# Optimization experiments

Hardware: AMD Instinct MI355X
Metric: run time of the kernel (lower is better)

Reference implementation:

```python
import jax, jax.numpy as jnp
import numpy as np

TEMPERATURE = 0.07
B, D = 8192, 256

def _l2norm(x, axis=-1, eps=1e-12):
    # matches torch F.normalize(p=2): x / max(||x||, eps)
    n = jnp.sqrt(jnp.sum(x * x, axis=axis, keepdims=True))
    return x / jnp.maximum(n, eps)

def setup_inputs() -> dict:
    key = jax.random.key(0)
    k1, k2, k3 = jax.random.split(key, 3)
    return {
        "h_emb": jax.random.normal(k1, (B, D), dtype=jnp.float32),
        "r_emb": jax.random.normal(k2, (B, D), dtype=jnp.float32),
        "t_emb": jax.random.normal(k3, (B, D), dtype=jnp.float32),
    }

def reference(h_emb, r_emb, t_emb):
    # query = normalize(h + r); positives/negatives = normalize(t)
    q = _l2norm(h_emb + r_emb, axis=1)          # [B, D]
    t = _l2norm(t_emb, axis=1)                  # [B, D]
    # Dense in-batch similarity. The original builds logits = [pos, off-diag negs];
    # since the diagonal of sim IS the positive similarity, cross-entropy with
    # label 0 equals logsumexp over the full row minus the diagonal entry.
    sim = jnp.einsum('bd,nd->bn', q, t) / TEMPERATURE   # [B, B]
    pos = jnp.diagonal(sim)                              # [B]
    loss = jnp.mean(jax.nn.logsumexp(sim, axis=1) - pos)
    return loss
```

## Files before the change

### kernel.cpp

```cpp
#include <hip/hip_runtime.h>
#include <hip/hip_bf16.h>

#define B_DIM 8192
#define D_DIM 256
#define GRID_GEMM 512
#define NT 16

constexpr float INV_T = 14.285714285714286f;

typedef __bf16 bf16x8 __attribute__((ext_vector_type(8)));
typedef float  f32x16 __attribute__((ext_vector_type(16)));

#define GLOBAL_U32(p) ((const __attribute__((address_space(1))) unsigned int*)(p))
#define LDS_U32(p)    ((__attribute__((address_space(3))) unsigned int*)(p))

#define WAITCNT_VM8 0x0F78

__device__ inline unsigned short f2bf(float f) {
    union { float f; unsigned u; } x; x.f = f;
    unsigned r = x.u + 0x7fffu + ((x.u >> 16) & 1u);
    return (unsigned short)(r >> 16);
}

__global__ __launch_bounds__(256) void norm_kernel(
    const float* __restrict__ h, const float* __restrict__ r,
    const float* __restrict__ t,
    unsigned short* __restrict__ qws, unsigned short* __restrict__ tws,
    float* __restrict__ rowsum, float* __restrict__ diagsum, int* __restrict__ ticket)
{
    if (blockIdx.x == 0) {
        float4* rs4 = (float4*)rowsum;
#pragma unroll
        for (int i = 0; i < 8; ++i)
            rs4[threadIdx.x * 8 + i] = make_float4(0.f, 0.f, 0.f, 0.f);
        if (threadIdx.x == 0) { *diagsum = 0.f; *ticket = 0; }
    }

    int wave = threadIdx.x >> 6;
    int lane = threadIdx.x & 63;
    int task = blockIdx.x * 4 + wave;
    bool isQ = task < B_DIM;
    int row  = isQ ? task : task - B_DIM;

    float4 v;
    if (isQ) {
        float4 a = ((const float4*)h)[row * 64 + lane];
        float4 b = ((const float4*)r)[row * 64 + lane];
        v = make_float4(a.x + b.x, a.y + b.y, a.z + b.z, a.w + b.w);
    } else {
        v = ((const float4*)t)[row * 64 + lane];
    }
    float s = v.x * v.x + v.y * v.y + v.z * v.z + v.w * v.w;
#pragma unroll
    for (int off = 32; off; off >>= 1) s += __shfl_xor(s, off, 64);
    float scale = 1.0f / fmaxf(sqrtf(s), 1e-12f);

    ushort4 o;
    o.x = f2bf(v.x * scale);
    o.y = f2bf(v.y * scale);
    o.z = f2bf(v.z * scale);
    o.w = f2bf(v.w * scale);
    ushort4* dst = (ushort4*)(isQ ? qws : tws);
    dst[row * 64 + lane] = o;
}

__global__ __launch_bounds__(256, 2) void gemm_lse_kernel(
    const unsigned char* __restrict__ qws, const unsigned char* __restrict__ tws,
    float* __restrict__ rowsum, float* __restrict__ diagsum,
    int* __restrict__ ticket, float* __restrict__ out)
{
    __shared__ __align__(16) unsigned char ldsB[4][32 * 512];
    __shared__ float wred[4];
    __shared__ int lastflag;

    const int tid  = threadIdx.x;
    const int lane = tid & 63;
    const int w    = tid >> 6;
    const int l31  = lane & 31;
    const int hi   = lane >> 5;

    const int cc   = blockIdx.x & 15;
    const int rb   = blockIdx.x >> 4;
    const int row0 = rb * 256 + w * 64;
    const int col0 = cc * 512;

    int srel[4];
#pragma unroll
    for (int it = 0; it < 4; ++it) {
        int s = it * 256 + tid;
        int n = s >> 5;
        int kc = (s & 31) ^ (n & 7);
        srel[it] = n * 512 + kc * 16;
    }

#define STAGE(snt, bufi)                                                     \
    {                                                                        \
        const unsigned char* gs = tws + (size_t)(col0 + (snt) * 32) * 512;   \
        _Pragma("unroll")                                                    \
        for (int it = 0; it < 4; ++it)                                       \
            __builtin_amdgcn_global_load_lds(                                \
                GLOBAL_U32(gs + srel[it]),                                   \
                LDS_U32(&ldsB[bufi][(it * 256 + tid) * 16]), 16, 0, 0);      \
    }

    STAGE(0, 0);
    STAGE(1, 1);

    bf16x8 a[2][16];
    {
        const unsigned char* abase = qws + (size_t)(row0 + l31) * 512 + hi * 16;
#pragma unroll
        for (int rt = 0; rt < 2; ++rt)
#pragma unroll
            for (int ks = 0; ks < 16; ++ks)
                a[rt][ks] = *(const bf16x8*)(abase + rt * (32 * 512) + ks * 32);
    }

    f32x16 rowacc[2] = {};
    float diagacc = 0.f;
    const int nsw = l31 & 7;

    for (int nt = 0; nt < NT; ++nt) {
        const int snt = (nt + 2 < NT) ? nt + 2 : NT - 1;
        STAGE(snt, (nt + 2) & 3);

        __builtin_amdgcn_s_waitcnt(WAITCNT_VM8);
        __builtin_amdgcn_s_barrier();

        const unsigned char* bbuf = ldsB[nt & 3];
        f32x16 acc0 = {}, acc1 = {};
#pragma unroll
        for (int ks = 0; ks < 16; ++ks) {
            int kc = ks * 2 + hi;
            bf16x8 b = *(const bf16x8*)(bbuf + l31 * 512 + ((kc ^ nsw) * 16));
            acc0 = __builtin_amdgcn_mfma_f32_32x32x16_bf16(a[0][ks], b, acc0, 0, 0, 0);
            acc1 = __builtin_amdgcn_mfma_f32_32x32x16_bf16(a[1][ks], b, acc1, 0, 0, 0);
        }

#pragma unroll
        for (int g = 0; g < 16; ++g) {
            rowacc[0][g] += __expf(fmaf(acc0[g], INV_T, -INV_T));
            rowacc[1][g] += __expf(fmaf(acc1[g], INV_T, -INV_T));
        }

        const int c0t = col0 + nt * 32;
        if (c0t == row0) {
#pragma unroll
            for (int g = 0; g < 16; ++g) {
                int rm = (g & 3) + 8 * (g >> 2) + 4 * hi;
                if (l31 == rm) diagacc += acc0[g] * INV_T;
            }
        }
        if (c0t == row0 + 32) {
#pragma unroll
            for (int g = 0; g < 16; ++g) {
                int rm = (g & 3) + 8 * (g >> 2) + 4 * hi;
                if (l31 == rm) diagacc += acc1[g] * INV_T;
            }
        }
    }

#pragma unroll
    for (int rt = 0; rt < 2; ++rt)
#pragma unroll
        for (int g = 0; g < 16; ++g) {
            float s = rowacc[rt][g];
            s += __shfl_xor(s, 1, 64);
            s += __shfl_xor(s, 2, 64);
            s += __shfl_xor(s, 4, 64);
            s += __shfl_xor(s, 8, 64);
            s += __shfl_xor(s, 16, 64);
            if (l31 == 0) {
                int grow = row0 + rt * 32 + (g & 3) + 8 * (g >> 2) + 4 * hi;
                atomicAdd(&rowsum[grow], s);
            }
        }

    float dsum = diagacc;
#pragma unroll
    for (int off = 32; off; off >>= 1) dsum += __shfl_xor(dsum, off, 64);
    if (lane == 0 && dsum != 0.f) atomicAdd(diagsum, dsum);

    __syncthreads();
    if (tid == 0) {
        __threadfence();
        int old = __hip_atomic_fetch_add(ticket, 1, __ATOMIC_ACQ_REL,
                                         __HIP_MEMORY_SCOPE_AGENT);
        lastflag = (old == GRID_GEMM - 1);
    }
    __syncthreads();
    if (!lastflag) return;

    float lsum = 0.f;
    for (int rr = tid; rr < B_DIM; rr += 256) {
        float rs = __hip_atomic_load(&rowsum[rr], __ATOMIC_RELAXED,
                                     __HIP_MEMORY_SCOPE_AGENT);
        lsum += __logf(rs);
    }
#pragma unroll
    for (int off = 32; off; off >>= 1) lsum += __shfl_xor(lsum, off, 64);
    if (lane == 0) wred[w] = lsum;
    __syncthreads();
    if (tid == 0) {
        float ds = __hip_atomic_load(diagsum, __ATOMIC_RELAXED,
                                     __HIP_MEMORY_SCOPE_AGENT);
        float total = wred[0] + wred[1] + wred[2] + wred[3]
                    + (float)B_DIM * INV_T
                    - ds;
        out[0] = total / (float)B_DIM;
    }
}

extern "C" void kernel_launch(void* const* d_in, const int* in_sizes, int n_in,
                              void* d_out, int out_size, void* d_ws, size_t ws_size,
                              hipStream_t stream)
{
    const float* h = (const float*)d_in[0];
    const float* r = (const float*)d_in[1];
    const float* t = (const float*)d_in[2];

    unsigned char* ws = (unsigned char*)d_ws;
    unsigned short* qws = (unsigned short*)ws;
    unsigned short* tws = (unsigned short*)(ws + 4u * 1024 * 1024);
    float* rowsum  = (float*)(ws + 8u * 1024 * 1024);
    float* diagsum = (float*)(ws + 8u * 1024 * 1024 + 32u * 1024);
    int*   ticket  = (int*)  (ws + 8u * 1024 * 1024 + 32u * 1024 + 16);

    norm_kernel<<<4096, 256, 0, stream>>>(h, r, t, qws, tws, rowsum, diagsum, ticket);
    gemm_lse_kernel<<<GRID_GEMM, 256, 0, stream>>>(
        (const unsigned char*)qws, (const unsigned char*)tws,
        rowsum, diagsum, ticket, (float*)d_out);
}
```

Measured before the change: 134.0 us.

## Software-pipeline exp epilogue behind next tile's MFMAs and coarsen norm kernel

The GEMM loop is restructured so that the exp/row-sum epilogue for tile n-1 is issued after the MFMAs for tile n, with ping-pong accumulators. This lets transcendental VALU work overlap matrix-core execution. s_setprio is also raised around the compute section. Separately, the norm kernel processes four rows per wave with a quarter of the blocks, cutting launch and block overhead. The cost is extra accumulator registers under a 2-blocks-per-CU launch bound, which could cause spills.

```diff
diff --git a/kernel.cpp b/kernel.cpp
--- a/kernel.cpp
+++ b/kernel.cpp
@@ -36,32 +36,36 @@
         if (threadIdx.x == 0) { *diagsum = 0.f; *ticket = 0; }
     }
 
-    int wave = threadIdx.x >> 6;
-    int lane = threadIdx.x & 63;
-    int task = blockIdx.x * 4 + wave;
-    bool isQ = task < B_DIM;
-    int row  = isQ ? task : task - B_DIM;
-
-    float4 v;
-    if (isQ) {
-        float4 a = ((const float4*)h)[row * 64 + lane];
-        float4 b = ((const float4*)r)[row * 64 + lane];
-        v = make_float4(a.x + b.x, a.y + b.y, a.z + b.z, a.w + b.w);
-    } else {
-        v = ((const float4*)t)[row * 64 + lane];
-    }
-    float s = v.x * v.x + v.y * v.y + v.z * v.z + v.w * v.w;
-#pragma unroll
-    for (int off = 32; off; off >>= 1) s += __shfl_xor(s, off, 64);
-    float scale = 1.0f / fmaxf(sqrtf(s), 1e-12f);
-
-    ushort4 o;
-    o.x = f2bf(v.x * scale);
-    o.y = f2bf(v.y * scale);
-    o.z = f2bf(v.z * scale);
-    o.w = f2bf(v.w * scale);
-    ushort4* dst = (ushort4*)(isQ ? qws : tws);
-    dst[row * 64 + lane] = o;
+    const int wave = threadIdx.x >> 6;
+    const int lane = threadIdx.x & 63;
+    const int wid  = blockIdx.x * 4 + wave;
+
+#pragma unroll
+    for (int k = 0; k < 4; ++k) {
+        const bool isQ = (k < 2);
+        const int row = wid + (k & 1) * 4096;
+
+        float4 v;
+        if (isQ) {
+            float4 a = ((const float4*)h)[row * 64 + lane];
+            float4 b = ((const float4*)r)[row * 64 + lane];
+            v = make_float4(a.x + b.x, a.y + b.y, a.z + b.z, a.w + b.w);
+        } else {
+            v = ((const float4*)t)[row * 64 + lane];
+        }
+        float s = v.x * v.x + v.y * v.y + v.z * v.z + v.w * v.w;
+#pragma unroll
+        for (int off = 32; off; off >>= 1) s += __shfl_xor(s, off, 64);
+        float scale = 1.0f / fmaxf(sqrtf(s), 1e-12f);
+
+        ushort4 o;
+        o.x = f2bf(v.x * scale);
+        o.y = f2bf(v.y * scale);
+        o.z = f2bf(v.z * scale);
+        o.w = f2bf(v.w * scale);
+        ushort4* dst = (ushort4*)(isQ ? qws : tws);
+        dst[row * 64 + lane] = o;
+    }
 }
 
 __global__ __launch_bounds__(256, 2) void gemm_lse_kernel(
@@ -120,51 +124,67 @@
     float diagacc = 0.f;
     const int nsw = l31 & 7;
 
-    for (int nt = 0; nt < NT; ++nt) {
-        const int snt = (nt + 2 < NT) ? nt + 2 : NT - 1;
-        STAGE(snt, (nt + 2) & 3);
-
-        __builtin_amdgcn_s_waitcnt(WAITCNT_VM8);
-        __builtin_amdgcn_s_barrier();
-
-        const unsigned char* bbuf = ldsB[nt & 3];
-        f32x16 acc0 = {}, acc1 = {};
-#pragma unroll
-        for (int ks = 0; ks < 16; ++ks) {
-            int kc = ks * 2 + hi;
-            bf16x8 b = *(const bf16x8*)(bbuf + l31 * 512 + ((kc ^ nsw) * 16));
-            acc0 = __builtin_amdgcn_mfma_f32_32x32x16_bf16(a[0][ks], b, acc0, 0, 0, 0);
-            acc1 = __builtin_amdgcn_mfma_f32_32x32x16_bf16(a[1][ks], b, acc1, 0, 0, 0);
-        }
-
+#define EPI(ntp, P0, P1)                                                     \
+    {                                                                        \
+        _Pragma("unroll")                                                    \
+        for (int g = 0; g < 16; ++g) {                                       \
+            rowacc[0][g] += __expf(fmaf(P0[g], INV_T, -INV_T));              \
+            rowacc[1][g] += __expf(fmaf(P1[g], INV_T, -INV_T));              \
+        }                                                                    \
+        const int c0p = col0 + (ntp) * 32;                                   \
+        if (c0p == row0) {                                                   \
+            _Pragma("unroll")                                                \
+            for (int g = 0; g < 16; ++g) {                                   \
+                const int rm = (g & 3) + 8 * (g >> 2) + 4 * hi;              \
+                if (l31 == rm) diagacc += P0[g] * INV_T;                     \
+            }                                                                \
+        }                                                                    \
+        if (c0p == row0 + 32) {                                              \
+            _Pragma("unroll")                                                \
+            for (int g = 0; g < 16; ++g) {                                   \
+                const int rm = (g & 3) + 8 * (g >> 2) + 4 * hi;              \
+                if (l31 == rm) diagacc += P1[g] * INV_T;                     \
+            }                                                                \
+        }                                                                    \
+    }
+
+#define ROUND(nt_, C0, C1, EPIST)                                            \
+    {                                                                        \
+        const int snt_ = ((nt_) + 2 < NT) ? (nt_) + 2 : NT - 1;              \
+        STAGE(snt_, ((nt_) + 2) & 3);                                        \
+        __builtin_amdgcn_s_waitcnt(WAITCNT_VM8);                             \
+        __builtin_amdgcn_s_barrier();                                        \
+        const unsigned char* bbuf_ = ldsB[(nt_) & 3];                        \
+        C0 = (f32x16){};                                                     \
+        C1 = (f32x16){};                                                     \
+        __builtin_amdgcn_s_setprio(1);                                       \
+        _Pragma("unroll")                                                    \
+        for (int ks = 0; ks < 16; ++ks) {                                    \
+            const int kc = ks * 2 + hi;                                      \
+            bf16x8 b = *(const bf16x8*)(bbuf_ + l31 * 512 + ((kc ^ nsw) * 16)); \
+            C0 = __builtin_amdgcn_mfma_f32_32x32x16_bf16(a[0][ks], b, C0, 0, 0, 0); \
+            C1 = __builtin_amdgcn_mfma_f32_32x32x16_bf16(a[1][ks], b, C1, 0, 0, 0); \
+        }                                                                    \
+        EPIST;                                                               \
+        __builtin_amdgcn_s_setprio(0);                                       \
+    }
+
+    f32x16 e0, e1, o0, o1;
+    ROUND(0, e0, e1, (void)0);
+#pragma unroll 1
+    for (int p = 0; p < 7; ++p) {
+        const int nt = 1 + 2 * p;
+        ROUND(nt,     o0, o1, EPI(nt - 1, e0, e1));
+        ROUND(nt + 1, e0, e1, EPI(nt,     o0, o1));
+    }
+    ROUND(15, o0, o1, EPI(14, e0, e1));
+    EPI(15, o0, o1);
+
+#pragma unroll
+    for (int rt = 0; rt < 2; ++rt)
 #pragma unroll
         for (int g = 0; g < 16; ++g) {
-            rowacc[0][g] += __expf(fmaf(acc0[g], INV_T, -INV_T));
-            rowacc[1][g] += __expf(fmaf(acc1[g], INV_T, -INV_T));
-        }
-
-        const int c0t = col0 + nt * 32;
-        if (c0t == row0) {
-#pragma unroll
-            for (int g = 0; g < 16; ++g) {
-                int rm = (g & 3) + 8 * (g >> 2) + 4 * hi;
-                if (l31 == rm) diagacc += acc0[g] * INV_T;
-            }
-        }
-        if (c0t == row0 + 32) {
-#pragma unroll
-            for (int g = 0; g < 16; ++g) {
-                int rm = (g & 3) + 8 * (g >> 2) + 4 * hi;
-                if (l31 == rm) diagacc += acc1[g] * INV_T;
-            }
-        }
-    }
-
-#pragma unroll
-    for (int rt = 0; rt < 2; ++rt)
-#pragma unroll
-        for (int g = 0; g < 16; ++g) {
-            float s = rowacc[rt][g];
+            float s = (rt == 0) ? rowacc[0][g] : rowacc[1][g];
             s += __shfl_xor(s, 1, 64);
             s += __shfl_xor(s, 2, 64);
             s += __shfl_xor(s, 4, 64);
@@ -226,7 +246,7 @@
     float* diagsum = (float*)(ws + 8u * 1024 * 1024 + 32u * 1024);
     int*   ticket  = (int*)  (ws + 8u * 1024 * 1024 + 32u * 1024 + 16);
 
-    norm_kernel<<<4096, 256, 0, stream>>>(h, r, t, qws, tws, rowsum, diagsum, ticket);
+    norm_kernel<<<1024, 256, 0, stream>>>(h, r, t, qws, tws, rowsum, diagsum, ticket);
     gemm_lse_kernel<<<GRID_GEMM, 256, 0, stream>>>(
         (const unsigned char*)qws, (const unsigned char*)tws,
         rowsum, diagsum, ticket, (float*)d_out);
```

Result: slower. 167.5 us (+25.0%).

## Fuse normalization into GEMM kernel with a grid-wide barrier

Applied to the files above, without the earlier changes.

Merges the normalization kernel into the GEMM+logsumexp kernel. Each of the 512 blocks first normalizes 16 q rows and 16 t rows, then all blocks meet at an atomic spin barrier before the GEMM phase. The accumulators are now zeroed with hipMemsetAsync, which replaces the launch-time zeroing that block 0 of the old normalization kernel did. This removes one kernel launch and the gap between the two kernels. The barrier relies on all 512 blocks being co-resident and adds a memset launch.

```diff
diff --git a/kernel.cpp b/kernel.cpp
--- a/kernel.cpp
+++ b/kernel.cpp
@@ -22,52 +22,12 @@
     return (unsigned short)(r >> 16);
 }
 
-__global__ __launch_bounds__(256) void norm_kernel(
+__global__ __launch_bounds__(256, 2) void fused_kernel(
     const float* __restrict__ h, const float* __restrict__ r,
     const float* __restrict__ t,
     unsigned short* __restrict__ qws, unsigned short* __restrict__ tws,
-    float* __restrict__ rowsum, float* __restrict__ diagsum, int* __restrict__ ticket)
-{
-    if (blockIdx.x == 0) {
-        float4* rs4 = (float4*)rowsum;
-#pragma unroll
-        for (int i = 0; i < 8; ++i)
-            rs4[threadIdx.x * 8 + i] = make_float4(0.f, 0.f, 0.f, 0.f);
-        if (threadIdx.x == 0) { *diagsum = 0.f; *ticket = 0; }
-    }
-
-    int wave = threadIdx.x >> 6;
-    int lane = threadIdx.x & 63;
-    int task = blockIdx.x * 4 + wave;
-    bool isQ = task < B_DIM;
-    int row  = isQ ? task : task - B_DIM;
-
-    float4 v;
-    if (isQ) {
-        float4 a = ((const float4*)h)[row * 64 + lane];
-        float4 b = ((const float4*)r)[row * 64 + lane];
-        v = make_float4(a.x + b.x, a.y + b.y, a.z + b.z, a.w + b.w);
-    } else {
-        v = ((const float4*)t)[row * 64 + lane];
-    }
-    float s = v.x * v.x + v.y * v.y + v.z * v.z + v.w * v.w;
-#pragma unroll
-    for (int off = 32; off; off >>= 1) s += __shfl_xor(s, off, 64);
-    float scale = 1.0f / fmaxf(sqrtf(s), 1e-12f);
-
-    ushort4 o;
-    o.x = f2bf(v.x * scale);
-    o.y = f2bf(v.y * scale);
-    o.z = f2bf(v.z * scale);
-    o.w = f2bf(v.w * scale);
-    ushort4* dst = (ushort4*)(isQ ? qws : tws);
-    dst[row * 64 + lane] = o;
-}
-
-__global__ __launch_bounds__(256, 2) void gemm_lse_kernel(
-    const unsigned char* __restrict__ qws, const unsigned char* __restrict__ tws,
     float* __restrict__ rowsum, float* __restrict__ diagsum,
-    int* __restrict__ ticket, float* __restrict__ out)
+    int* __restrict__ ticket, int* __restrict__ gbar, float* __restrict__ out)
 {
     __shared__ __align__(16) unsigned char ldsB[4][32 * 512];
     __shared__ float wred[4];
@@ -79,6 +39,50 @@
     const int l31  = lane & 31;
     const int hi   = lane >> 5;
 
+    {
+        const int wg = blockIdx.x * 4 + w;
+#pragma unroll
+        for (int i = 0; i < 4; ++i) {
+            const int row = wg * 4 + i;
+            float4 a4 = ((const float4*)h)[row * 64 + lane];
+            float4 b4 = ((const float4*)r)[row * 64 + lane];
+            float4 v = make_float4(a4.x + b4.x, a4.y + b4.y,
+                                   a4.z + b4.z, a4.w + b4.w);
+            float s = v.x * v.x + v.y * v.y + v.z * v.z + v.w * v.w;
+#pragma unroll
+            for (int off = 32; off; off >>= 1) s += __shfl_xor(s, off, 64);
+            float scale = 1.0f / fmaxf(sqrtf(s), 1e-12f);
+            ushort4 o;
+            o.x = f2bf(v.x * scale); o.y = f2bf(v.y * scale);
+            o.z = f2bf(v.z * scale); o.w = f2bf(v.w * scale);
+            ((ushort4*)qws)[row * 64 + lane] = o;
+        }
+#pragma unroll
+        for (int i = 0; i < 4; ++i) {
+            const int row = wg * 4 + i;
+            float4 v = ((const float4*)t)[row * 64 + lane];
+            float s = v.x * v.x + v.y * v.y + v.z * v.z + v.w * v.w;
+#pragma unroll
+            for (int off = 32; off; off >>= 1) s += __shfl_xor(s, off, 64);
+            float scale = 1.0f / fmaxf(sqrtf(s), 1e-12f);
+            ushort4 o;
+            o.x = f2bf(v.x * scale); o.y = f2bf(v.y * scale);
+            o.z = f2bf(v.z * scale); o.w = f2bf(v.w * scale);
+            ((ushort4*)tws)[row * 64 + lane] = o;
+        }
+    }
+
+    __threadfence();
+    __syncthreads();
+    if (tid == 0) {
+        __hip_atomic_fetch_add(gbar, 1, __ATOMIC_ACQ_REL,
+                               __HIP_MEMORY_SCOPE_AGENT);
+        while (__hip_atomic_load(gbar, __ATOMIC_ACQUIRE,
+                                 __HIP_MEMORY_SCOPE_AGENT) < GRID_GEMM)
+            __builtin_amdgcn_s_sleep(1);
+    }
+    __syncthreads();
+
     const int cc   = blockIdx.x & 15;
     const int rb   = blockIdx.x >> 4;
     const int row0 = rb * 256 + w * 64;
@@ -95,7 +99,8 @@
 
 #define STAGE(snt, bufi)                                                     \
     {                                                                        \
-        const unsigned char* gs = tws + (size_t)(col0 + (snt) * 32) * 512;   \
+        const unsigned char* gs = (const unsigned char*)tws                  \
+                                  + (size_t)(col0 + (snt) * 32) * 512;       \
         _Pragma("unroll")                                                    \
         for (int it = 0; it < 4; ++it)                                       \
             __builtin_amdgcn_global_load_lds(                                \
@@ -108,7 +113,8 @@
 
     bf16x8 a[2][16];
     {
-        const unsigned char* abase = qws + (size_t)(row0 + l31) * 512 + hi * 16;
+        const unsigned char* abase = (const unsigned char*)qws
+                                     + (size_t)(row0 + l31) * 512 + hi * 16;
 #pragma unroll
         for (int rt = 0; rt < 2; ++rt)
 #pragma unroll
@@ -225,9 +231,10 @@
     float* rowsum  = (float*)(ws + 8u * 1024 * 1024);
     float* diagsum = (float*)(ws + 8u * 1024 * 1024 + 32u * 1024);
     int*   ticket  = (int*)  (ws + 8u * 1024 * 1024 + 32u * 1024 + 16);
-
-    norm_kernel<<<4096, 256, 0, stream>>>(h, r, t, qws, tws, rowsum, diagsum, ticket);
-    gemm_lse_kernel<<<GRID_GEMM, 256, 0, stream>>>(
-        (const unsigned char*)qws, (const unsigned char*)tws,
-        rowsum, diagsum, ticket, (float*)d_out);
+    int*   gbar    = (int*)  (ws + 8u * 1024 * 1024 + 32u * 1024 + 32);
+
+    hipMemsetAsync(ws + 8u * 1024 * 1024, 0, 32u * 1024 + 64, stream);
+
+    fused_kernel<<<GRID_GEMM, 256, 0, stream>>>(
+        h, r, t, qws, tws, rowsum, diagsum, ticket, gbar, (float*)d_out);
 }
```

Result: slower. 204.4 us (+52.5%).

## Drop LDS staging of T tiles in GEMM and batch rows per wave in norm

Applied to the files above, without the earlier changes.

The GEMM kernel no longer stages the normalized T tiles into a 4-deep LDS ring with global_load_lds and per-tile barriers. Each wave now reads its B fragments straight from global memory and relies on the caches for reuse across the four waves of a block. The norm kernel launches a quarter as many blocks, and each wave processes two Q rows and two T rows. This removes LDS traffic and barrier synchronisation, but it exposes global-load latency with no explicit prefetch and multiplies L1/L2 requests by four. The norm kernel also keeps a leftover dead loop that breaks immediately.

```diff
diff --git a/kernel.cpp b/kernel.cpp
--- a/kernel.cpp
+++ b/kernel.cpp
@@ -10,11 +10,6 @@
 
 typedef __bf16 bf16x8 __attribute__((ext_vector_type(8)));
 typedef float  f32x16 __attribute__((ext_vector_type(16)));
-
-#define GLOBAL_U32(p) ((const __attribute__((address_space(1))) unsigned int*)(p))
-#define LDS_U32(p)    ((__attribute__((address_space(3))) unsigned int*)(p))
-
-#define WAITCNT_VM8 0x0F78
 
 __device__ inline unsigned short f2bf(float f) {
     union { float f; unsigned u; } x; x.f = f;
@@ -36,32 +31,55 @@
         if (threadIdx.x == 0) { *diagsum = 0.f; *ticket = 0; }
     }
 
-    int wave = threadIdx.x >> 6;
-    int lane = threadIdx.x & 63;
-    int task = blockIdx.x * 4 + wave;
-    bool isQ = task < B_DIM;
-    int row  = isQ ? task : task - B_DIM;
-
-    float4 v;
-    if (isQ) {
-        float4 a = ((const float4*)h)[row * 64 + lane];
-        float4 b = ((const float4*)r)[row * 64 + lane];
-        v = make_float4(a.x + b.x, a.y + b.y, a.z + b.z, a.w + b.w);
-    } else {
-        v = ((const float4*)t)[row * 64 + lane];
-    }
-    float s = v.x * v.x + v.y * v.y + v.z * v.z + v.w * v.w;
-#pragma unroll
-    for (int off = 32; off; off >>= 1) s += __shfl_xor(s, off, 64);
-    float scale = 1.0f / fmaxf(sqrtf(s), 1e-12f);
-
-    ushort4 o;
-    o.x = f2bf(v.x * scale);
-    o.y = f2bf(v.y * scale);
-    o.z = f2bf(v.z * scale);
-    o.w = f2bf(v.w * scale);
-    ushort4* dst = (ushort4*)(isQ ? qws : tws);
-    dst[row * 64 + lane] = o;
+    const int wave = threadIdx.x >> 6;
+    const int lane = threadIdx.x & 63;
+    const int wid  = blockIdx.x * 4 + wave;
+
+#pragma unroll
+    for (int k = 0; k < 4; ++k) {
+        const bool isQ = (k < 2);
+        const int row = wid * 2 + (k & 1) + (isQ ? 0 : 0);
+        const int rr  = wid * 2 + (k & 1);
+        float4 v;
+        if (isQ) {
+            float4 a = ((const float4*)h)[(size_t)rr * 64 * 4 / 4 + 0];
+            (void)a;
+        }
+        (void)row;
+        break;
+    }
+
+    {
+        const int wg = blockIdx.x * 4 + wave;
+#pragma unroll
+        for (int i = 0; i < 2; ++i) {
+            const int row = wg * 2 + i;
+            float4 a = ((const float4*)h)[row * 64 + lane];
+            float4 b = ((const float4*)r)[row * 64 + lane];
+            float4 v = make_float4(a.x + b.x, a.y + b.y, a.z + b.z, a.w + b.w);
+            float s = v.x * v.x + v.y * v.y + v.z * v.z + v.w * v.w;
+#pragma unroll
+            for (int off = 32; off; off >>= 1) s += __shfl_xor(s, off, 64);
+            float scale = 1.0f / fmaxf(sqrtf(s), 1e-12f);
+            ushort4 o;
+            o.x = f2bf(v.x * scale); o.y = f2bf(v.y * scale);
+            o.z = f2bf(v.z * scale); o.w = f2bf(v.w * scale);
+            ((ushort4*)qws)[row * 64 + lane] = o;
+        }
+#pragma unroll
+        for (int i = 0; i < 2; ++i) {
+            const int row = wg * 2 + i;
+            float4 v = ((const float4*)t)[row * 64 + lane];
+            float s = v.x * v.x + v.y * v.y + v.z * v.z + v.w * v.w;
+#pragma unroll
+            for (int off = 32; off; off >>= 1) s += __shfl_xor(s, off, 64);
+            float scale = 1.0f / fmaxf(sqrtf(s), 1e-12f);
+            ushort4 o;
+            o.x = f2bf(v.x * scale); o.y = f2bf(v.y * scale);
+            o.z = f2bf(v.z * scale); o.w = f2bf(v.w * scale);
+            ((ushort4*)tws)[row * 64 + lane] = o;
+        }
+    }
 }
 
 __global__ __launch_bounds__(256, 2) void gemm_lse_kernel(
@@ -69,7 +87,6 @@
     float* __restrict__ rowsum, float* __restrict__ diagsum,
     int* __restrict__ ticket, float* __restrict__ out)
 {
-    __shared__ __align__(16) unsigned char ldsB[4][32 * 512];
     __shared__ float wred[4];
     __shared__ int lastflag;
 
@@ -84,28 +101,6 @@
     const int row0 = rb * 256 + w * 64;
     const int col0 = cc * 512;
 
-    int srel[4];
-#pragma unroll
-    for (int it = 0; it < 4; ++it) {
-        int s = it * 256 + tid;
-        int n = s >> 5;
-        int kc = (s & 31) ^ (n & 7);
-        srel[it] = n * 512 + kc * 16;
-    }
-
-#define STAGE(snt, bufi)                                                     \
-    {                                                                        \
-        const unsigned char* gs = tws + (size_t)(col0 + (snt) * 32) * 512;   \
-        _Pragma("unroll")                                                    \
-        for (int it = 0; it < 4; ++it)                                       \
-            __builtin_amdgcn_global_load_lds(                                \
-                GLOBAL_U32(gs + srel[it]),                                   \
-                LDS_U32(&ldsB[bufi][(it * 256 + tid) * 16]), 16, 0, 0);      \
-    }
-
-    STAGE(0, 0);
-    STAGE(1, 1);
-
     bf16x8 a[2][16];
     {
         const unsigned char* abase = qws + (size_t)(row0 + l31) * 512 + hi * 16;
@@ -118,21 +113,14 @@
 
     f32x16 rowacc[2] = {};
     float diagacc = 0.f;
-    const int nsw = l31 & 7;
 
     for (int nt = 0; nt < NT; ++nt) {
-        const int snt = (nt + 2 < NT) ? nt + 2 : NT - 1;
-        STAGE(snt, (nt + 2) & 3);
-
-        __builtin_amdgcn_s_waitcnt(WAITCNT_VM8);
-        __builtin_amdgcn_s_barrier();
-
-        const unsigned char* bbuf = ldsB[nt & 3];
+        const unsigned char* bb = tws + (size_t)(col0 + nt * 32 + l31) * 512 + hi * 16;
+
         f32x16 acc0 = {}, acc1 = {};
 #pragma unroll
         for (int ks = 0; ks < 16; ++ks) {
-            int kc = ks * 2 + hi;
-            bf16x8 b = *(const bf16x8*)(bbuf + l31 * 512 + ((kc ^ nsw) * 16));
+            bf16x8 b = *(const bf16x8*)(bb + ks * 32);
             acc0 = __builtin_amdgcn_mfma_f32_32x32x16_bf16(a[0][ks], b, acc0, 0, 0, 0);
             acc1 = __builtin_amdgcn_mfma_f32_32x32x16_bf16(a[1][ks], b, acc1, 0, 0, 0);
         }
@@ -226,7 +214,7 @@
     float* diagsum = (float*)(ws + 8u * 1024 * 1024 + 32u * 1024);
     int*   ticket  = (int*)  (ws + 8u * 1024 * 1024 + 32u * 1024 + 16);
 
-    norm_kernel<<<4096, 256, 0, stream>>>(h, r, t, qws, tws, rowsum, diagsum, ticket);
+    norm_kernel<<<1024, 256, 0, stream>>>(h, r, t, qws, tws, rowsum, diagsum, ticket);
     gemm_lse_kernel<<<GRID_GEMM, 256, 0, stream>>>(
         (const unsigned char*)qws, (const unsigned char*)tws,
         rowsum, diagsum, ticket, (float*)d_out);
```

Measured after the change: 167.0 us. 24.6% more time.
